# Optimization experiments

Measured on AMD Instinct MI355X. Metric: run time of the kernel, lower is better.

## Reference

```python
import jax, jax.numpy as jnp
import numpy as np

N_HEAD = 16

def setup_inputs() -> dict:
    key = jax.random.key(0)
    k1, k2, k3 = jax.random.split(key, 3)
    B, S, D = 2, 2048, 1024
    std = 0.02
    return {
        "hidden_states": jax.random.normal(k1, (B, S, D), jnp.float32),
        "w_attn": jax.random.normal(k2, (D, 3 * D), jnp.float32) * std,
        "b_attn": jnp.zeros((3 * D,), jnp.float32),
        "w_proj": jax.random.normal(k3, (D, D), jnp.float32) * std,
        "b_proj": jnp.zeros((D,), jnp.float32),
    }

def reference(hidden_states, w_attn, b_attn, w_proj, b_proj):
    B, S, D = hidden_states.shape
    H = N_HEAD
    hd = D // H
    # fused qkv projection (Conv1D == x @ W + b)
    qkv = hidden_states @ w_attn + b_attn            # [B,S,3D]
    q, k, v = jnp.split(qkv, 3, axis=-1)
    def split_heads(t):
        return t.reshape(B, S, H, hd).transpose(0, 2, 1, 3)  # [B,H,S,hd]
    q, k, v = split_heads(q), split_heads(k), split_heads(v)
    # scores with scale = sqrt(head_dim)
    scores = jnp.einsum('bhqd,bhkd->bhqk', q, k) / jnp.sqrt(jnp.asarray(hd, q.dtype))
    causal = jnp.tril(jnp.ones((S, S), bool))
    mask_value = jnp.finfo(scores.dtype).min
    scores = jnp.where(causal, scores, mask_value)
    attn = jax.nn.softmax(scores, axis=-1)           # dropout p=0 (eval)
    out = jnp.einsum('bhqk,bhkd->bhqd', attn, v)     # [B,H,S,hd]
    out = out.transpose(0, 2, 1, 3).reshape(B, S, D)
    out = out @ w_proj + b_proj
    return out
```

## Files before the change

### kernel.cpp

```cpp
#include <hip/hip_runtime.h>

#define S_LEN 2048
#define D_MODEL 1024
#define NHEAD 16
#define HDIM 64
#define BATCH 2
#define M_ROWS (BATCH * S_LEN)
#define N_QKV (3 * D_MODEL)
#define QSCALE 0.18033688011112042f

typedef __attribute__((ext_vector_type(8))) short bf16x8;
typedef __attribute__((ext_vector_type(4))) short bf16x4;
typedef __attribute__((ext_vector_type(4))) float f32x4;

#if __has_builtin(__builtin_amdgcn_mfma_f32_16x16x16bf16_1k)
#define MFMA1616(A, B, C) __builtin_amdgcn_mfma_f32_16x16x16bf16_1k((A), (B), (C), 0, 0, 0)
#else
static __device__ __forceinline__ f32x4 mfma1616_asm(bf16x4 a, bf16x4 b, f32x4 c) {
  asm("v_mfma_f32_16x16x16_bf16 %0, %1, %2, %0" : "+v"(c) : "v"(a), "v"(b));
  return c;
}
#define MFMA1616(A, B, C) mfma1616_asm((A), (B), (C))
#endif

static __device__ __forceinline__ unsigned short f2bf(float f) {
  unsigned int u = __float_as_uint(f);
  u += 0x7FFFu + ((u >> 16) & 1u);
  return (unsigned short)(u >> 16);
}
static __device__ __forceinline__ unsigned int pkbf(float a, float b) {
  unsigned int ua = __float_as_uint(a) + 0x8000u;
  unsigned int ub = __float_as_uint(b) + 0x8000u;
  return __builtin_amdgcn_perm(ub, ua, 0x07060302u);
}

static __device__ __forceinline__ void async_cp16(unsigned short* lds, const unsigned short* g) {
  __builtin_amdgcn_global_load_lds((__attribute__((address_space(1))) void*)g,
                                   (__attribute__((address_space(3))) void*)lds, 16, 0, 0);
}

__global__ __launch_bounds__(256) void k_prep(const float* __restrict__ x,
                                              unsigned short* __restrict__ xb,
                                              const float* __restrict__ w_attn,
                                              unsigned short* __restrict__ wqkvT,
                                              const float* __restrict__ w_proj,
                                              unsigned short* __restrict__ wprojT) {
  __shared__ unsigned short T[32][33];
  const int blk = blockIdx.x;
  const int tid = threadIdx.x;
  if (blk < 4096) {
    int i = blk * 256 + tid;
    float4 v = ((const float4*)x)[i];
    ushort4 o;
    o.x = f2bf(v.x); o.y = f2bf(v.y); o.z = f2bf(v.z); o.w = f2bf(v.w);
    ((ushort4*)xb)[i] = o;
    return;
  }
  const float* w;
  unsigned short* wT;
  int bid, Ndim;
  if (blk < 7168) { bid = blk - 4096; w = w_attn; wT = wqkvT; Ndim = N_QKV; }
  else            { bid = blk - 7168; w = w_proj; wT = wprojT; Ndim = D_MODEL; }
  const int nb = Ndim / 32;
  const int n0 = (bid % nb) * 32, k0 = (bid / nb) * 32;
  const int tx = tid & 31, ty = tid >> 5;
#pragma unroll
  for (int j = 0; j < 4; ++j) {
    int r = ty + j * 8;
    T[r][tx] = f2bf(w[(size_t)(k0 + r) * Ndim + n0 + tx]);
  }
  __syncthreads();
#pragma unroll
  for (int j = 0; j < 4; ++j) {
    int r = ty + j * 8;
    wT[(size_t)(n0 + r) * D_MODEL + k0 + tx] = T[tx][r];
  }
}

__global__ __launch_bounds__(256) void k_gemm_qkv(const unsigned short* __restrict__ A,
                                                  const unsigned short* __restrict__ Bt,
                                                  const float* __restrict__ bias,
                                                  unsigned short* __restrict__ Qb,
                                                  unsigned short* __restrict__ Kbuf,
                                                  unsigned short* __restrict__ VTb) {
  __shared__ __align__(16) unsigned short As[2][128 * 32];
  __shared__ __align__(16) unsigned short Bs[2][128 * 32];
  const int tid = threadIdx.x;
  const int wid = tid >> 6, lane = tid & 63;
  const int lr = lane & 15, lg = lane >> 4;
  const int blk = blockIdx.x;
  const int xcd = blk & 7, idx = blk >> 3;
  const int bm = ((xcd & 3) * 8 + (idx & 7)) * 128;
  const int bn = ((xcd >> 2) * 12 + (idx >> 3)) * 128;
  const int wm = (wid >> 1) * 64, wn = (wid & 1) * 64;
  const int K = D_MODEL;
  const int c0 = tid, c1 = tid + 256;
  const size_t a0o = (size_t)(bm + (c0 >> 2)) * K + (c0 & 3) * 8;
  const size_t a1o = (size_t)(bm + (c1 >> 2)) * K + (c1 & 3) * 8;
  const size_t b0o = (size_t)(bn + (c0 >> 2)) * K + (c0 & 3) * 8;
  const size_t b1o = (size_t)(bn + (c1 >> 2)) * K + (c1 & 3) * 8;

  f32x4 acc[4][4] = {};

  async_cp16(&As[0][c0 * 8], &A[a0o]);
  async_cp16(&As[0][c1 * 8], &A[a1o]);
  async_cp16(&Bs[0][c0 * 8], &Bt[b0o]);
  async_cp16(&Bs[0][c1 * 8], &Bt[b1o]);

  for (int k0 = 0; k0 < K; k0 += 32) {
    const int p = (k0 >> 5) & 1;
    __syncthreads();
    if (k0 + 32 < K) {
      async_cp16(&As[p ^ 1][c0 * 8], &A[a0o + k0 + 32]);
      async_cp16(&As[p ^ 1][c1 * 8], &A[a1o + k0 + 32]);
      async_cp16(&Bs[p ^ 1][c0 * 8], &Bt[b0o + k0 + 32]);
      async_cp16(&Bs[p ^ 1][c1 * 8], &Bt[b1o + k0 + 32]);
    }
    bf16x8 af[4], bfr[4];
#pragma unroll
    for (int i = 0; i < 4; ++i) af[i] = *(const bf16x8*)&As[p][(wm + i * 16 + lr) * 32 + lg * 8];
#pragma unroll
    for (int t = 0; t < 4; ++t) bfr[t] = *(const bf16x8*)&Bs[p][(wn + t * 16 + lr) * 32 + lg * 8];
#pragma unroll
    for (int i = 0; i < 4; ++i)
#pragma unroll
      for (int t = 0; t < 4; ++t)
        acc[i][t] = __builtin_amdgcn_mfma_f32_16x16x32_bf16(af[i], bfr[t], acc[i][t], 0, 0, 0);
  }
#pragma unroll
  for (int i = 0; i < 4; ++i) {
#pragma unroll
    for (int t = 0; t < 4; ++t) {
      int n = bn + wn + t * 16 + lr;
      int part = n >> 10, rem = n & 1023;
      int h = rem >> 6, d = rem & 63;
      float bv = bias[n];
      int row0 = bm + wm + i * 16 + lg * 4;
      int bb = row0 >> 11, s0 = row0 & 2047;
      if (part == 2) {
        ushort4 vv;
        vv.x = f2bf(acc[i][t][0] + bv);
        vv.y = f2bf(acc[i][t][1] + bv);
        vv.z = f2bf(acc[i][t][2] + bv);
        vv.w = f2bf(acc[i][t][3] + bv);
        *(ushort4*)&VTb[(((size_t)(bb << 4) + h) * HDIM + d) * S_LEN + s0] = vv;
      } else {
        unsigned short* dst = (part == 0) ? Qb : Kbuf;
        float sc = (part == 0) ? QSCALE : 1.0f;
#pragma unroll
        for (int r = 0; r < 4; ++r)
          dst[(((size_t)(bb << 4) + h) * S_LEN + (s0 + r)) * HDIM + d] = f2bf((acc[i][t][r] + bv) * sc);
      }
    }
  }
}

__global__ __launch_bounds__(256) void k_gemm_proj(const unsigned short* __restrict__ A,
                                                   const unsigned short* __restrict__ Bt,
                                                   const float* __restrict__ bias,
                                                   float* __restrict__ out) {
  __shared__ __align__(16) unsigned short As[2][128 * 32];
  __shared__ __align__(16) unsigned short Bs[2][128 * 32];
  const int tid = threadIdx.x;
  const int wid = tid >> 6, lane = tid & 63;
  const int lr = lane & 15, lg = lane >> 4;
  const int blk = blockIdx.x;
  const int xcd = blk & 7, idx = blk >> 3;
  const int bm = (xcd * 4 + (idx & 3)) * 128;
  const int bn = (idx >> 2) * 128;
  const int wm = (wid >> 1) * 64, wn = (wid & 1) * 64;
  const int K = D_MODEL;
  const int c0 = tid, c1 = tid + 256;
  const size_t a0o = (size_t)(bm + (c0 >> 2)) * K + (c0 & 3) * 8;
  const size_t a1o = (size_t)(bm + (c1 >> 2)) * K + (c1 & 3) * 8;
  const size_t b0o = (size_t)(bn + (c0 >> 2)) * K + (c0 & 3) * 8;
  const size_t b1o = (size_t)(bn + (c1 >> 2)) * K + (c1 & 3) * 8;

  f32x4 acc[4][4] = {};

  async_cp16(&As[0][c0 * 8], &A[a0o]);
  async_cp16(&As[0][c1 * 8], &A[a1o]);
  async_cp16(&Bs[0][c0 * 8], &Bt[b0o]);
  async_cp16(&Bs[0][c1 * 8], &Bt[b1o]);

  for (int k0 = 0; k0 < K; k0 += 32) {
    const int p = (k0 >> 5) & 1;
    __syncthreads();
    if (k0 + 32 < K) {
      async_cp16(&As[p ^ 1][c0 * 8], &A[a0o + k0 + 32]);
      async_cp16(&As[p ^ 1][c1 * 8], &A[a1o + k0 + 32]);
      async_cp16(&Bs[p ^ 1][c0 * 8], &Bt[b0o + k0 + 32]);
      async_cp16(&Bs[p ^ 1][c1 * 8], &Bt[b1o + k0 + 32]);
    }
    bf16x8 af[4], bfr[4];
#pragma unroll
    for (int i = 0; i < 4; ++i) af[i] = *(const bf16x8*)&As[p][(wm + i * 16 + lr) * 32 + lg * 8];
#pragma unroll
    for (int t = 0; t < 4; ++t) bfr[t] = *(const bf16x8*)&Bs[p][(wn + t * 16 + lr) * 32 + lg * 8];
#pragma unroll
    for (int i = 0; i < 4; ++i)
#pragma unroll
      for (int t = 0; t < 4; ++t)
        acc[i][t] = __builtin_amdgcn_mfma_f32_16x16x32_bf16(af[i], bfr[t], acc[i][t], 0, 0, 0);
  }
#pragma unroll
  for (int i = 0; i < 4; ++i) {
#pragma unroll
    for (int t = 0; t < 4; ++t) {
      int n = bn + wn + t * 16 + lr;
      float bv = bias[n];
#pragma unroll
      for (int r = 0; r < 4; ++r) {
        int row = bm + wm + i * 16 + lg * 4 + r;
        out[(size_t)row * D_MODEL + n] = acc[i][t][r] + bv;
      }
    }
  }
}

__global__ __launch_bounds__(256, 4) void k_attn8(const unsigned short* __restrict__ Qb,
                                                  const unsigned short* __restrict__ Kb,
                                                  const unsigned short* __restrict__ VT,
                                                  unsigned short* __restrict__ AO) {
  const int tid = threadIdx.x;
  const int wid = tid >> 6, lane = tid & 63;
  const int lr = lane & 15, quad = lane >> 4;
  const int blk = blockIdx.x;
  const int bh = blk & 31;
  const int g = blk >> 5;
  const int b = bh >> 4, h = bh & 15;
  const int sL = (g < 16) ? (g * 4 + wid) : (127 - ((g - 16) * 4 + wid));
  const int R = sL * 16;
  const int ntile = (sL >> 2) + 1;

  __shared__ __align__(16) unsigned short Ks[2][64 * 64];
  __shared__ __align__(16) unsigned short Vs[2][64 * 64];

  const unsigned short* Kbh = Kb + (size_t)bh * S_LEN * HDIM;
  const unsigned short* VTbh = VT + (size_t)bh * HDIM * S_LEN;

  bf16x8 qf[2];
#pragma unroll
  for (int dh = 0; dh < 2; ++dh)
    qf[dh] = *(const bf16x8*)&Qb[((size_t)bh * S_LEN + R + lr) * HDIM + dh * 32 + quad * 8];

  f32x4 Ot[4] = {};
  float ms = -1e30f;
  float ls = 0.f;

  const int srow = lane >> 3;
  const int scol = ((lane & 7) ^ srow) * 8;

#pragma unroll
  for (int j = 0; j < 2; ++j) {
    const int r0 = wid * 16 + j * 8;
    async_cp16(&Ks[0][r0 * 64 + lane * 8], &Kbh[(size_t)(r0 + srow) * HDIM + scol]);
    async_cp16(&Vs[0][r0 * 64 + lane * 8], &VTbh[(size_t)(r0 + srow) * S_LEN + scol]);
  }

  for (int kt = 0; kt < ntile; ++kt) {
    const int k0 = kt * 64;
    const int p = kt & 1;
    __syncthreads();
    if (kt + 1 < ntile) {
      const int kn = k0 + 64;
#pragma unroll
      for (int j = 0; j < 2; ++j) {
        const int r0 = wid * 16 + j * 8;
        async_cp16(&Ks[p ^ 1][r0 * 64 + lane * 8], &Kbh[(size_t)(kn + r0 + srow) * HDIM + scol]);
        async_cp16(&Vs[p ^ 1][r0 * 64 + lane * 8], &VTbh[(size_t)(r0 + srow) * S_LEN + kn + scol]);
      }
    }

    bf16x8 kf[4][2];
#pragma unroll
    for (int kg = 0; kg < 4; ++kg)
#pragma unroll
      for (int dh = 0; dh < 2; ++dh)
        kf[kg][dh] = *(const bf16x8*)&Ks[p][(kg * 16 + lr) * 64 + (((dh * 4 + quad) ^ (lr & 7)) * 8)];

    f32x4 Sv[4];
#pragma unroll
    for (int kg = 0; kg < 4; ++kg) {
      f32x4 a = {};
      a = __builtin_amdgcn_mfma_f32_16x16x32_bf16(kf[kg][0], qf[0], a, 0, 0, 0);
      a = __builtin_amdgcn_mfma_f32_16x16x32_bf16(kf[kg][1], qf[1], a, 0, 0, 0);
      Sv[kg] = a;
    }
    if (k0 + 63 > R) {
      const int q = R + lr;
#pragma unroll
      for (int kg = 0; kg < 4; ++kg)
#pragma unroll
        for (int r = 0; r < 4; ++r)
          if (k0 + kg * 16 + quad * 4 + r > q) Sv[kg][r] = -1e30f;
    }
    float mx = ms;
#pragma unroll
    for (int kg = 0; kg < 4; ++kg)
      mx = fmaxf(mx, fmaxf(fmaxf(Sv[kg][0], Sv[kg][1]), fmaxf(Sv[kg][2], Sv[kg][3])));
    mx = fmaxf(mx, __shfl_xor(mx, 16));
    mx = fmaxf(mx, __shfl_xor(mx, 32));
    const float alpha = __builtin_amdgcn_exp2f(ms - mx);
    ms = mx;
    bf16x4 pf[4];
    float rs = 0.f;
#pragma unroll
    for (int kg = 0; kg < 4; ++kg) {
      float e0 = __builtin_amdgcn_exp2f(Sv[kg][0] - mx);
      float e1 = __builtin_amdgcn_exp2f(Sv[kg][1] - mx);
      float e2 = __builtin_amdgcn_exp2f(Sv[kg][2] - mx);
      float e3 = __builtin_amdgcn_exp2f(Sv[kg][3] - mx);
      rs += (e0 + e1) + (e2 + e3);
      union { bf16x4 v; unsigned int u[2]; } pu;
      pu.u[0] = pkbf(e0, e1);
      pu.u[1] = pkbf(e2, e3);
      pf[kg] = pu.v;
    }
    rs += __shfl_xor(rs, 16);
    rs += __shfl_xor(rs, 32);
    ls = ls * alpha + rs;
#pragma unroll
    for (int dg = 0; dg < 4; ++dg)
#pragma unroll
      for (int r = 0; r < 4; ++r) Ot[dg][r] *= alpha;

#pragma unroll
    for (int dg = 0; dg < 4; ++dg) {
      bf16x4 vf[4];
#pragma unroll
      for (int kg = 0; kg < 4; ++kg)
        vf[kg] = *(const bf16x4*)&Vs[p][(dg * 16 + lr) * 64 +
                                        (((kg * 2 + (quad >> 1)) ^ (lr & 7)) * 8) + (quad & 1) * 4];
#pragma unroll
      for (int kg = 0; kg < 4; ++kg)
        Ot[dg] = MFMA1616(vf[kg], pf[kg], Ot[dg]);
    }
  }

  const float rl = __builtin_amdgcn_rcpf(ls);
  const int s = R + lr;
#pragma unroll
  for (int dg = 0; dg < 4; ++dg) {
    const size_t o = ((size_t)b * S_LEN + s) * D_MODEL + h * 64 + dg * 16 + quad * 4;
    *(unsigned int*)&AO[o]     = pkbf(Ot[dg][0] * rl, Ot[dg][1] * rl);
    *(unsigned int*)&AO[o + 2] = pkbf(Ot[dg][2] * rl, Ot[dg][3] * rl);
  }
}

extern "C" void kernel_launch(void* const* d_in, const int* in_sizes, int n_in,
                              void* d_out, int out_size, void* d_ws, size_t ws_size,
                              hipStream_t stream) {
  const float* x      = (const float*)d_in[0];
  const float* w_attn = (const float*)d_in[1];
  const float* b_attn = (const float*)d_in[2];
  const float* w_proj = (const float*)d_in[3];
  const float* b_proj = (const float*)d_in[4];
  float* out = (float*)d_out;

  unsigned short* ws     = (unsigned short*)d_ws;
  unsigned short* xb     = ws;
  unsigned short* wqkvT  = xb + (size_t)M_ROWS * D_MODEL;
  unsigned short* wprojT = wqkvT + (size_t)N_QKV * D_MODEL;
  unsigned short* Qb     = wprojT + (size_t)D_MODEL * D_MODEL;
  unsigned short* Kb     = Qb + (size_t)M_ROWS * D_MODEL;
  unsigned short* VT     = Kb + (size_t)M_ROWS * D_MODEL;
  unsigned short* AO     = xb;

  k_prep<<<8192, 256, 0, stream>>>(x, xb, w_attn, wqkvT, w_proj, wprojT);
  k_gemm_qkv<<<768, 256, 0, stream>>>(xb, wqkvT, b_attn, Qb, Kb, VT);
  k_attn8<<<1024, 256, 0, stream>>>(Qb, Kb, VT, AO);
  k_gemm_proj<<<256, 256, 0, stream>>>(AO, wprojT, b_proj, out);
}
```

Before: 181.6 us.

## Split long causal attention rows into two KV chunks with a combine kernel

```diff
diff --git a/kernel.cpp b/kernel.cpp
--- a/kernel.cpp
+++ b/kernel.cpp
@@ -218,20 +218,31 @@
   }
 }
 
-__global__ __launch_bounds__(256, 4) void k_attn8(const unsigned short* __restrict__ Qb,
+__global__ __launch_bounds__(256, 5) void k_attn9(const unsigned short* __restrict__ Qb,
                                                   const unsigned short* __restrict__ Kb,
                                                   const unsigned short* __restrict__ VT,
-                                                  unsigned short* __restrict__ AO) {
+                                                  unsigned short* __restrict__ AO,
+                                                  float* __restrict__ Pp) {
   const int tid = threadIdx.x;
   const int wid = tid >> 6, lane = tid & 63;
   const int lr = lane & 15, quad = lane >> 4;
   const int blk = blockIdx.x;
   const int bh = blk & 31;
-  const int g = blk >> 5;
+  const int id = blk >> 5;
   const int b = bh >> 4, h = bh & 15;
-  const int sL = (g < 16) ? (g * 4 + wid) : (127 - ((g - 16) * 4 + wid));
+
+  int t, c;
+  if (id < 17)       { t = 31 - id; c = 0; }
+  else if (id == 17) { t = 31;      c = 1; }
+  else {
+    const int k = id - 18, p_ = k >> 1;
+    if (k & 1) { t = 30 - p_; c = 1; }
+    else       { t = 14 - p_; c = 0; }
+  }
+  const int sL = t * 4 + wid;
   const int R = sL * 16;
-  const int ntile = (sL >> 2) + 1;
+  const int kt0 = c << 4;
+  const int ktend = (c == 0) ? ((t + 1 < 16) ? (t + 1) : 16) : (t + 1);
 
   __shared__ __align__(16) unsigned short Ks[2][64 * 64];
   __shared__ __align__(16) unsigned short Vs[2][64 * 64];
@@ -251,18 +262,21 @@
   const int srow = lane >> 3;
   const int scol = ((lane & 7) ^ srow) * 8;
 
-#pragma unroll
-  for (int j = 0; j < 2; ++j) {
-    const int r0 = wid * 16 + j * 8;
-    async_cp16(&Ks[0][r0 * 64 + lane * 8], &Kbh[(size_t)(r0 + srow) * HDIM + scol]);
-    async_cp16(&Vs[0][r0 * 64 + lane * 8], &VTbh[(size_t)(r0 + srow) * S_LEN + scol]);
-  }
-
-  for (int kt = 0; kt < ntile; ++kt) {
+  {
+    const int kg0 = kt0 * 64;
+#pragma unroll
+    for (int j = 0; j < 2; ++j) {
+      const int r0 = wid * 16 + j * 8;
+      async_cp16(&Ks[0][r0 * 64 + lane * 8], &Kbh[(size_t)(kg0 + r0 + srow) * HDIM + scol]);
+      async_cp16(&Vs[0][r0 * 64 + lane * 8], &VTbh[(size_t)(r0 + srow) * S_LEN + kg0 + scol]);
+    }
+  }
+
+  for (int kt = kt0; kt < ktend; ++kt) {
     const int k0 = kt * 64;
     const int p = kt & 1;
     __syncthreads();
-    if (kt + 1 < ntile) {
+    if (kt + 1 < ktend) {
       const int kn = k0 + 64;
 #pragma unroll
       for (int j = 0; j < 2; ++j) {
@@ -338,13 +352,51 @@
     }
   }
 
-  const float rl = __builtin_amdgcn_rcpf(ls);
-  const int s = R + lr;
-#pragma unroll
-  for (int dg = 0; dg < 4; ++dg) {
-    const size_t o = ((size_t)b * S_LEN + s) * D_MODEL + h * 64 + dg * 16 + quad * 4;
-    *(unsigned int*)&AO[o]     = pkbf(Ot[dg][0] * rl, Ot[dg][1] * rl);
-    *(unsigned int*)&AO[o + 2] = pkbf(Ot[dg][2] * rl, Ot[dg][3] * rl);
+  if (t < 16) {
+    const float rl = __builtin_amdgcn_rcpf(ls);
+    const int s = R + lr;
+#pragma unroll
+    for (int dg = 0; dg < 4; ++dg) {
+      const size_t o = ((size_t)b * S_LEN + s) * D_MODEL + h * 64 + dg * 16 + quad * 4;
+      *(unsigned int*)&AO[o]     = pkbf(Ot[dg][0] * rl, Ot[dg][1] * rl);
+      *(unsigned int*)&AO[o + 2] = pkbf(Ot[dg][2] * rl, Ot[dg][3] * rl);
+    }
+  } else {
+    float* P = Pp + ((size_t)((bh * 64 + (sL - 64)) * 2 + c)) * (16 * 68) + lr * 68;
+#pragma unroll
+    for (int dg = 0; dg < 4; ++dg)
+      *(f32x4*)&P[dg * 16 + quad * 4] = Ot[dg];
+    if (quad == 0) { P[64] = ms; P[65] = ls; }
+  }
+}
+
+__global__ __launch_bounds__(256) void k_combine(const float* __restrict__ Pp,
+                                                 unsigned short* __restrict__ AO) {
+  const int lane = threadIdx.x & 63;
+  const int sid = blockIdx.x * 4 + (threadIdx.x >> 6);
+  const int bh = sid >> 6, jrel = sid & 63;
+  const int b = bh >> 4, h = bh & 15;
+  const int r = lane & 15, cg = lane >> 4;
+  const float* P0 = Pp + ((size_t)(bh * 64 + jrel) * 2) * (16 * 68) + r * 68;
+  const float* P1 = P0 + 16 * 68;
+  const float m0 = P0[64], l0 = P0[65];
+  const float m1 = P1[64], l1 = P1[65];
+  const float M = fmaxf(m0, m1);
+  const float w0 = __builtin_amdgcn_exp2f(m0 - M);
+  const float w1 = __builtin_amdgcn_exp2f(m1 - M);
+  const float rl = __builtin_amdgcn_rcpf(l0 * w0 + l1 * w1);
+  const int s = (64 + jrel) * 16 + r;
+  const size_t o0 = ((size_t)b * S_LEN + s) * D_MODEL + h * 64 + cg * 16;
+#pragma unroll
+  for (int q4 = 0; q4 < 4; ++q4) {
+    f32x4 a = *(const f32x4*)&P0[cg * 16 + q4 * 4];
+    f32x4 b4 = *(const f32x4*)&P1[cg * 16 + q4 * 4];
+    float o0v = (a[0] * w0 + b4[0] * w1) * rl;
+    float o1v = (a[1] * w0 + b4[1] * w1) * rl;
+    float o2v = (a[2] * w0 + b4[2] * w1) * rl;
+    float o3v = (a[3] * w0 + b4[3] * w1) * rl;
+    *(unsigned int*)&AO[o0 + q4 * 4]     = pkbf(o0v, o1v);
+    *(unsigned int*)&AO[o0 + q4 * 4 + 2] = pkbf(o2v, o3v);
   }
 }
 
@@ -365,10 +417,12 @@
   unsigned short* Qb     = wprojT + (size_t)D_MODEL * D_MODEL;
   unsigned short* Kb     = Qb + (size_t)M_ROWS * D_MODEL;
   unsigned short* VT     = Kb + (size_t)M_ROWS * D_MODEL;
+  float* Pp              = (float*)(VT + (size_t)M_ROWS * D_MODEL);
   unsigned short* AO     = xb;
 
   k_prep<<<8192, 256, 0, stream>>>(x, xb, w_attn, wqkvT, w_proj, wprojT);
   k_gemm_qkv<<<768, 256, 0, stream>>>(xb, wqkvT, b_attn, Qb, Kb, VT);
-  k_attn8<<<1024, 256, 0, stream>>>(Qb, Kb, VT, AO);
+  k_attn9<<<1536, 256, 0, stream>>>(Qb, Kb, VT, AO, Pp);
+  k_combine<<<512, 256, 0, stream>>>(Pp, AO);
   k_gemm_proj<<<256, 256, 0, stream>>>(AO, wprojT, b_proj, out);
 }
```

Result: no change. 180.5 us (-0.6%).
